# Kernel optimization log

Measured on AMD Instinct MI355X. Metric: run time of the kernel, lower is better.

The kernel has to match this reference:

```python
import jax, jax.numpy as jnp
import numpy as np

B, T, D, H = 4, 2048, 1024, 16
HD = D // H  # head_dim = 64


def setup_inputs() -> dict:
    key = jax.random.key(0)
    k1, k2, k3 = jax.random.split(key, 3)
    s = 0.02
    return {
        "x": jax.random.normal(k1, (B, T, D), dtype=jnp.float32),
        "qkv_w": jax.random.normal(k2, (D, 3 * D), dtype=jnp.float32) * s,
        "qkv_b": jnp.zeros((3 * D,), dtype=jnp.float32),
        "proj_w": jax.random.normal(k3, (D, D), dtype=jnp.float32) * s,
        "proj_b": jnp.zeros((D,), dtype=jnp.float32),
    }


def reference(x, qkv_w, qkv_b, proj_w, proj_b):
    b, t, d = x.shape
    qkv = x @ qkv_w + qkv_b                       # [B,T,3D]
    q, k, v = jnp.split(qkv, 3, axis=-1)
    # [B,T,D] -> [B,H,T,hd]
    q = q.reshape(b, t, H, HD).transpose(0, 2, 1, 3)
    k = k.reshape(b, t, H, HD).transpose(0, 2, 1, 3)
    v = v.reshape(b, t, H, HD).transpose(0, 2, 1, 3)
    att = jnp.einsum("bhqd,bhkd->bhqk", q, k) / np.sqrt(HD).astype(np.float32)
    causal = jnp.tril(jnp.ones((t, t), dtype=bool))
    att = jnp.where(causal[None, None], att, jnp.finfo(att.dtype).min)
    att = jax.nn.softmax(att, axis=-1)
    out = jnp.einsum("bhqk,bhkd->bhqd", att, v)   # [B,H,T,hd]
    out = out.transpose(0, 2, 1, 3).reshape(b, t, H * HD)
    out = out @ proj_w + proj_b                   # dropout p=0.0 -> identity
    return out
```

## Files before the change

kernel.cpp:

```cpp
#include <hip/hip_runtime.h>
#include <hip/hip_bf16.h>

#define Bsz 4
#define Tsz 2048
#define Dsz 1024
#define Hsz 16
#define HDsz 64

typedef __attribute__((ext_vector_type(8))) __bf16 bf16x8;
typedef __attribute__((ext_vector_type(4))) __bf16 bf16x4;
typedef __attribute__((ext_vector_type(4))) float f32x4;
typedef __attribute__((ext_vector_type(2))) float f32x2;
typedef unsigned short u16;
typedef unsigned int u32;

#define DEVI static __device__ __forceinline__

DEVI u16 f2bf(float f) {
    __bf16 h = (__bf16)f;
    union { __bf16 h; u16 u; } c; c.h = h; return c.u;
}
DEVI bf16x8 ld_bf8(const u16* p) { return *reinterpret_cast<const bf16x8*>(p); }

DEVI void gll16(const u16* g, u16* lds) {
    __builtin_amdgcn_global_load_lds(
        (const __attribute__((address_space(1))) u32*)g,
        (__attribute__((address_space(3))) u32*)lds, 16, 0, 0);
}

DEVI void mfma16(f32x4& c, f32x2 a, f32x2 b) {
    asm("v_mfma_f32_16x16x16_bf16 %0, %1, %2, %0" : "+v"(c) : "v"(a), "v"(b));
}

__global__ __launch_bounds__(256)
void conv_bf16(const float* __restrict__ X, u16* __restrict__ Xb)
{
    const size_t i = ((size_t)blockIdx.x * 256 + threadIdx.x) * 8;
    const float4 a = *(const float4*)(X + i);
    const float4 b = *(const float4*)(X + i + 4);
    u16 h[8] = { f2bf(a.x), f2bf(a.y), f2bf(a.z), f2bf(a.w),
                 f2bf(b.x), f2bf(b.y), f2bf(b.z), f2bf(b.w) };
    *(uint4*)(Xb + i) = *(uint4*)h;
}

__global__ __launch_bounds__(256)
void transpose_w(const float* __restrict__ W, u16* __restrict__ WT, int K, int N)
{
    __shared__ float tile[64][65];
    const int n0 = blockIdx.x * 64, k0 = blockIdx.y * 64;
    const int t = threadIdx.x;
    #pragma unroll
    for (int i = 0; i < 4; ++i) {
        const int idx = i*256 + t;
        const int row = idx >> 4, c4 = (idx & 15) * 4;
        const float4 v = *(const float4*)(W + (size_t)(k0 + row)*N + n0 + c4);
        tile[row][c4+0] = v.x; tile[row][c4+1] = v.y;
        tile[row][c4+2] = v.z; tile[row][c4+3] = v.w;
    }
    __syncthreads();
    #pragma unroll
    for (int j = 0; j < 2; ++j) {
        const int idx = j*256 + t;
        const int nr = idx >> 3, kc = (idx & 7) * 8;
        u16 h[8];
        #pragma unroll
        for (int e = 0; e < 8; ++e) h[e] = f2bf(tile[kc + e][nr]);
        *(uint4*)(WT + (size_t)(n0 + nr)*K + k0 + kc) = *(uint4*)h;
    }
}

template<int EPI>
__global__ __launch_bounds__(256, 3)
void gemm128(const u16* __restrict__ A, const u16* __restrict__ Bt,
             const float* __restrict__ bias, float* __restrict__ Cf,
             u16* __restrict__ Qo, u16* __restrict__ Ko, u16* __restrict__ Vo,
             int M, int N, int K)
{
    __shared__ u16 As[3][128][32];
    __shared__ u16 Bs[3][128][32];

    const int nx  = N >> 7;
    const int nwg = (int)gridDim.x;
    const int cpx = nwg >> 3;
    const int orig = blockIdx.x;
    const int bid  = (orig & 7) * cpx + (orig >> 3);
    const int tN = bid % nx, tM = bid / nx;

    const int t = threadIdx.x, l = t & 63, w = t >> 6;
    const int wm = w >> 1, wn = w & 1;
    const int lrow = l & 15, lk = l >> 4;

    f32x4 acc[4][4] = {};

    const u16* Ag = A  + (size_t)tM * 128 * K;
    const u16* Bg = Bt + (size_t)tN * 128 * K;

    int srow[2], sch[2];
    #pragma unroll
    for (int r = 0; r < 2; ++r) {
        const int c = r*256 + t;
        srow[r] = c >> 2;
        sch[r]  = (c & 3) ^ ((srow[r] >> 1) & 3);
    }
    const size_t ldso = (size_t)(t & 192) * 8;

    #define STAGE(buf, ks)                                                      \
        {                                                                       \
            _Pragma("unroll")                                                   \
            for (int r = 0; r < 2; ++r) {                                       \
                gll16(Ag + (size_t)srow[r]*K + (ks) + sch[r]*8,                 \
                      &As[buf][0][0] + (size_t)r*2048 + ldso);                  \
                gll16(Bg + (size_t)srow[r]*K + (ks) + sch[r]*8,                 \
                      &Bs[buf][0][0] + (size_t)r*2048 + ldso);                  \
            }                                                                   \
        }

    STAGE(0, 0);
    STAGE(1, 32);

    const int nk = K >> 5;
    int cur = 0;
    for (int i = 0; i < nk; ++i) {
        asm volatile("s_waitcnt vmcnt(4)" ::: "memory");
        __builtin_amdgcn_sched_barrier(0);
        __builtin_amdgcn_s_barrier();

        bf16x8 a[4], bb[4];
        #pragma unroll
        for (int ii = 0; ii < 4; ++ii) {
            const int ar = wm*64 + ii*16 + lrow;
            a[ii] = ld_bf8(&As[cur][ar][(lk ^ ((ar >> 1) & 3)) * 8]);
        }
        #pragma unroll
        for (int j = 0; j < 4; ++j) {
            const int br = wn*64 + j*16 + lrow;
            bb[j] = ld_bf8(&Bs[cur][br][(lk ^ ((br >> 1) & 3)) * 8]);
        }

        if (i + 2 < nk) {
            const int nb = (cur + 2) - ((cur + 2) >= 3 ? 3 : 0);
            STAGE(nb, (i + 2) * 32);
        }

        __builtin_amdgcn_s_setprio(1);
        #pragma unroll
        for (int ii = 0; ii < 4; ++ii)
        #pragma unroll
        for (int j = 0; j < 4; ++j)
            acc[ii][j] = __builtin_amdgcn_mfma_f32_16x16x32_bf16(a[ii], bb[j], acc[ii][j], 0, 0, 0);
        __builtin_amdgcn_s_setprio(0);

        cur = (cur + 1) - ((cur + 1) >= 3 ? 3 : 0);
    }
    #undef STAGE

    #pragma unroll
    for (int i = 0; i < 4; ++i)
    #pragma unroll
    for (int j = 0; j < 4; ++j)
    #pragma unroll
    for (int r = 0; r < 4; ++r) {
        const int row = tM*128 + wm*64 + i*16 + lk*4 + r;
        const int col = tN*128 + wn*64 + j*16 + lrow;
        const float v = acc[i][j][r] + bias[col];
        if (EPI == 0) {
            Cf[(size_t)row * N + col] = v;
        } else {
            const int which = col >> 10;
            const int h  = (col & 1023) >> 6;
            const int hd = col & 63;
            const int b  = row >> 11;
            const int tt = row & 2047;
            const int bh = b * Hsz + h;
            const u16 bv = f2bf(v);
            if (which == 0)      Qo[((size_t)bh * Tsz + tt) * HDsz + hd] = bv;
            else if (which == 1) Ko[((size_t)bh * Tsz + tt) * HDsz + hd] = bv;
            else                 Vo[((size_t)bh * HDsz + hd) * Tsz + tt] = bv;
        }
    }
}

__global__ __launch_bounds__(256, 4)
void attn3(const u16* __restrict__ Q, const u16* __restrict__ K,
           const u16* __restrict__ Vt, u16* __restrict__ AO)
{
    __shared__ u16 KV[2][2][64][64];

    const int y = blockIdx.y;
    const int x = blockIdx.x;
    const int idx = (x + (y >> 4)) & 15;
    const int qt = (idx & 1) ? (idx >> 1) : (15 - (idx >> 1));
    const int bh = y;
    const int t = threadIdx.x, w = t >> 6, l = t & 63;
    const int lrow = l & 15, lk = l >> 4;
    const int qw = qt*128 + w*32;
    const int qwmax = qw + 31;
    const int swz = lrow & 7;

    const u16* Qh = Q  + (size_t)bh * Tsz * HDsz;
    const u16* Kh = K  + (size_t)bh * Tsz * HDsz;
    const u16* Vh = Vt + (size_t)bh * HDsz * Tsz;

    bf16x8 qf[2][2];
    #pragma unroll
    for (int f = 0; f < 2; ++f)
    #pragma unroll
    for (int kh = 0; kh < 2; ++kh)
        qf[f][kh] = ld_bf8(&Qh[(size_t)(qw + f*16 + lrow)*HDsz + kh*32 + lk*8]);

    f32x4 o[2][4] = {};
    float m[2] = {-3e38f, -3e38f}, lsum[2] = {0.f, 0.f};

    const int ntile = 2*qt + 2;
    int cur = 0;

    #pragma unroll
    for (int rr = 0; rr < 2; ++rr) {
        const int c = rr*256 + t;
        const int row = c >> 3, gc = (c & 7) ^ (row & 7);
        gll16(Kh + (size_t)row*HDsz + gc*8,
              &KV[0][0][0][0] + (size_t)(rr*256 + (t & 192))*8);
        gll16(Vh + (size_t)row*Tsz + gc*8,
              &KV[0][1][0][0] + (size_t)(rr*256 + (t & 192))*8);
    }
    __syncthreads();

    for (int tk = 0; tk < ntile; ++tk) {
        if (tk + 1 < ntile) {
            const int nkv = (tk + 1) * 64;
            #pragma unroll
            for (int rr = 0; rr < 2; ++rr) {
                const int c = rr*256 + t;
                const int row = c >> 3, gc = (c & 7) ^ (row & 7);
                gll16(Kh + (size_t)(nkv + row)*HDsz + gc*8,
                      &KV[cur^1][0][0][0] + (size_t)(rr*256 + (t & 192))*8);
                gll16(Vh + (size_t)row*Tsz + nkv + gc*8,
                      &KV[cur^1][1][0][0] + (size_t)(rr*256 + (t & 192))*8);
            }
        }
        const int kv0 = tk * 64;
        if (kv0 <= qwmax) {
            const u16 (*Ks)[64] = KV[cur][0];
            const u16 (*Vs)[64] = KV[cur][1];
            const bool fullc    = (kv0 + 63 <= qwmax);
            const bool needmask = (kv0 + 63 > qw);

            f32x4 s[2][4];
            __builtin_amdgcn_s_setprio(1);
            #pragma unroll
            for (int c = 0; c < 4; ++c) {
                if (c >= 2 && !fullc) continue;
                const bf16x8 k0 = ld_bf8(&Ks[c*16 + lrow][((0 + lk) ^ swz) * 8]);
                const bf16x8 k1 = ld_bf8(&Ks[c*16 + lrow][((4 + lk) ^ swz) * 8]);
                #pragma unroll
                for (int f = 0; f < 2; ++f) {
                    f32x4 z = {};
                    z = __builtin_amdgcn_mfma_f32_16x16x32_bf16(k0, qf[f][0], z, 0, 0, 0);
                    z = __builtin_amdgcn_mfma_f32_16x16x32_bf16(k1, qf[f][1], z, 0, 0, 0);
                    s[f][c] = z;
                }
            }
            __builtin_amdgcn_s_setprio(0);

            #pragma unroll
            for (int f = 0; f < 2; ++f) {
                const int q = qw + f*16 + lrow;
                if (needmask) {
                    #pragma unroll
                    for (int c = 0; c < 4; ++c) {
                        if (c >= 2 && !fullc) continue;
                        const int base = kv0 + c*16 + lk*4;
                        #pragma unroll
                        for (int r = 0; r < 4; ++r)
                            if (base + r > q) s[f][c][r] = -1e30f;
                    }
                }
                f32x4 t01;
                #pragma unroll
                for (int r = 0; r < 4; ++r) {
                    t01[r] = fmaxf(s[f][0][r], s[f][1][r]);
                    if (fullc) t01[r] = fmaxf(t01[r], fmaxf(s[f][2][r], s[f][3][r]));
                }
                float mx = fmaxf(fmaxf(t01[0], t01[1]), fmaxf(t01[2], t01[3]));
                mx = fmaxf(mx, __shfl_xor(mx, 16));
                mx = fmaxf(mx, __shfl_xor(mx, 32));
                if (__any(mx > m[f] + 64.f)) {
                    const float mn = fmaxf(m[f], mx);
                    const float al = __expf((m[f] - mn) * 0.125f);
                    lsum[f] *= al;
                    m[f] = mn;
                    #pragma unroll
                    for (int c = 0; c < 4; ++c)
                    #pragma unroll
                    for (int r = 0; r < 4; ++r) o[f][c][r] *= al;
                }
                const float nm8 = -m[f] * 0.125f;
                f32x4 ps4 = {};
                #pragma unroll
                for (int c = 0; c < 4; ++c) {
                    if (c >= 2 && !fullc) continue;
                    #pragma unroll
                    for (int r = 0; r < 4; ++r) {
                        const float p = __expf(fmaf(s[f][c][r], 0.125f, nm8));
                        s[f][c][r] = p;
                        ps4[r] += p;
                    }
                }
                float ps = (ps4[0] + ps4[1]) + (ps4[2] + ps4[3]);
                ps += __shfl_xor(ps, 16);
                ps += __shfl_xor(ps, 32);
                lsum[f] += ps;
            }

            __builtin_amdgcn_s_setprio(1);
            #pragma unroll
            for (int c = 0; c < 4; ++c) {
                if (c >= 2 && !fullc) continue;
                union { bf16x4 v; f32x2 f; } p0, p1;
                #pragma unroll
                for (int r = 0; r < 4; ++r) {
                    p0.v[r] = (__bf16)s[0][c][r];
                    p1.v[r] = (__bf16)s[1][c][r];
                }
                #pragma unroll
                for (int chd = 0; chd < 4; ++chd) {
                    const f32x2 va = *reinterpret_cast<const f32x2*>(
                        &Vs[chd*16 + lrow][(((c*2 + (lk >> 1)) ^ swz) << 3) + ((lk & 1) << 2)]);
                    mfma16(o[0][chd], va, p0.f);
                    mfma16(o[1][chd], va, p1.f);
                }
            }
            __builtin_amdgcn_s_setprio(0);
        }
        __syncthreads();
        cur ^= 1;
    }

    const int b = bh >> 4, h = bh & 15;
    #pragma unroll
    for (int f = 0; f < 2; ++f) {
        const float rl = 1.0f / lsum[f];
        #pragma unroll
        for (int chd = 0; chd < 4; ++chd) {
            u16 ov[4] = { f2bf(o[f][chd][0]*rl), f2bf(o[f][chd][1]*rl),
                          f2bf(o[f][chd][2]*rl), f2bf(o[f][chd][3]*rl) };
            *(ushort4*)(AO + ((size_t)(b*Tsz + qw + f*16 + lrow))*Dsz
                           + h*HDsz + chd*16 + lk*4) = *(ushort4*)ov;
        }
    }
}

extern "C" void kernel_launch(void* const* d_in, const int* in_sizes, int n_in,
                              void* d_out, int out_size, void* d_ws, size_t ws_size,
                              hipStream_t stream)
{
    (void)in_sizes; (void)n_in; (void)out_size; (void)ws_size;

    const float* x      = (const float*)d_in[0];
    const float* qkv_w  = (const float*)d_in[1];
    const float* qkv_b  = (const float*)d_in[2];
    const float* proj_w = (const float*)d_in[3];
    const float* proj_b = (const float*)d_in[4];
    float* out = (float*)d_out;

    char* ws = (char*)d_ws;
    const size_t SZ = (size_t)Bsz * Hsz * Tsz * HDsz * sizeof(u16);
    u16* R0 = (u16*)(ws);
    u16* Qb = (u16*)(ws + SZ);
    u16* Kb = (u16*)(ws + 2*SZ);
    u16* Vt = (u16*)(ws + 3*SZ);
    u16* WQKVT = R0;
    u16* AO    = R0;
    u16* WPT   = Qb;

    u16* Xb = (u16*)d_out;

    const int M = Bsz * Tsz;

    conv_bf16<<<(M*Dsz)/(256*8), 256, 0, stream>>>(x, Xb);
    transpose_w<<<dim3(3*Dsz/64, Dsz/64), 256, 0, stream>>>(qkv_w, WQKVT, Dsz, 3*Dsz);
    gemm128<1><<<dim3((3*Dsz/128) * (M/128)), 256, 0, stream>>>(
        Xb, WQKVT, qkv_b, nullptr, Qb, Kb, Vt, M, 3*Dsz, Dsz);
    attn3<<<dim3(Tsz/128, Bsz*Hsz), 256, 0, stream>>>(Qb, Kb, Vt, AO);
    transpose_w<<<dim3(Dsz/64, Dsz/64), 256, 0, stream>>>(proj_w, WPT, Dsz, Dsz);
    gemm128<0><<<dim3((Dsz/128) * (M/128)), 256, 0, stream>>>(
        AO, WPT, proj_b, out, nullptr, nullptr, nullptr, M, Dsz, Dsz);
}
```

Baseline: 201.6 us.

## Replace 128x128 GEMM with 256x256 tiled 8-wave GEMM using ping-pong quadrant schedule

Both projection GEMMs now use 256x256 output tiles with 512 threads (8 waves, 2x4 layout), a K-step of 64, and double-buffered LDS split into row halves. The main loop is split into four quadrant phases, with barriers between them and global-to-LDS prefetches spread across the phases, so loads overlap MFMA work. The aim is to raise arithmetic intensity and cut global and LDS traffic per FLOP. In exchange, the grid shrinks (only 128 blocks for the output projection, fewer than the CU count), register pressure rises, and there are more barriers per iteration.

```diff
diff --git a/kernel.cpp b/kernel.cpp
--- a/kernel.cpp
+++ b/kernel.cpp
@@ -70,98 +70,177 @@
 }
 
 template<int EPI>
-__global__ __launch_bounds__(256, 3)
-void gemm128(const u16* __restrict__ A, const u16* __restrict__ Bt,
+__global__ __launch_bounds__(512, 2)
+void gemm256(const u16* __restrict__ A, const u16* __restrict__ Bt,
              const float* __restrict__ bias, float* __restrict__ Cf,
              u16* __restrict__ Qo, u16* __restrict__ Ko, u16* __restrict__ Vo,
              int M, int N, int K)
 {
-    __shared__ u16 As[3][128][32];
-    __shared__ u16 Bs[3][128][32];
-
-    const int nx  = N >> 7;
+    __shared__ u16 Ash[2][2][128*64];
+    __shared__ u16 Bsh[2][2][128*64];
+
+    const int nx  = N >> 8;
     const int nwg = (int)gridDim.x;
     const int cpx = nwg >> 3;
-    const int orig = blockIdx.x;
+    const int orig = (int)blockIdx.x;
     const int bid  = (orig & 7) * cpx + (orig >> 3);
     const int tN = bid % nx, tM = bid / nx;
 
-    const int t = threadIdx.x, l = t & 63, w = t >> 6;
-    const int wm = w >> 1, wn = w & 1;
+    const int t = (int)threadIdx.x, l = t & 63, w = t >> 6;
+    const int wm = w >> 2, wn = w & 3;
     const int lrow = l & 15, lk = l >> 4;
 
-    f32x4 acc[4][4] = {};
-
-    const u16* Ag = A  + (size_t)tM * 128 * K;
-    const u16* Bg = Bt + (size_t)tN * 128 * K;
-
-    int srow[2], sch[2];
+    f32x4 acc[8][4] = {};
+
+    const u16* Ag = A  + (size_t)tM * 256 * K;
+    const u16* Bg = Bt + (size_t)tN * 256 * K;
+
+    int strow[2], scol[2];
     #pragma unroll
     for (int r = 0; r < 2; ++r) {
-        const int c = r*256 + t;
-        srow[r] = c >> 2;
-        sch[r]  = (c & 3) ^ ((srow[r] >> 1) & 3);
-    }
-    const size_t ldso = (size_t)(t & 192) * 8;
-
-    #define STAGE(buf, ks)                                                      \
-        {                                                                       \
-            _Pragma("unroll")                                                   \
-            for (int r = 0; r < 2; ++r) {                                       \
-                gll16(Ag + (size_t)srow[r]*K + (ks) + sch[r]*8,                 \
-                      &As[buf][0][0] + (size_t)r*2048 + ldso);                  \
-                gll16(Bg + (size_t)srow[r]*K + (ks) + sch[r]*8,                 \
-                      &Bs[buf][0][0] + (size_t)r*2048 + ldso);                  \
-            }                                                                   \
-        }
-
-    STAGE(0, 0);
-    STAGE(1, 32);
-
-    const int nk = K >> 5;
-    int cur = 0;
-    for (int i = 0; i < nk; ++i) {
-        asm volatile("s_waitcnt vmcnt(4)" ::: "memory");
-        __builtin_amdgcn_sched_barrier(0);
-        __builtin_amdgcn_s_barrier();
-
-        bf16x8 a[4], bb[4];
-        #pragma unroll
-        for (int ii = 0; ii < 4; ++ii) {
-            const int ar = wm*64 + ii*16 + lrow;
-            a[ii] = ld_bf8(&As[cur][ar][(lk ^ ((ar >> 1) & 3)) * 8]);
-        }
-        #pragma unroll
-        for (int j = 0; j < 4; ++j) {
-            const int br = wn*64 + j*16 + lrow;
-            bb[j] = ld_bf8(&Bs[cur][br][(lk ^ ((br >> 1) & 3)) * 8]);
-        }
-
-        if (i + 2 < nk) {
-            const int nb = (cur + 2) - ((cur + 2) >= 3 ? 3 : 0);
-            STAGE(nb, (i + 2) * 32);
-        }
-
+        const int c = r*512 + t;
+        strow[r] = c >> 3;
+        scol[r]  = (((c & 7) ^ ((strow[r] >> 1) & 7)) << 3);
+    }
+    const size_t ldso = (size_t)(t & 448) * 8;
+
+#define STG(buf, isB, half, kt) {                                              \
+    const u16* g0_ = (isB ? Bg : Ag) + ((size_t)(half)*128 + strow[0])*K + (kt) + scol[0]; \
+    const u16* g1_ = (isB ? Bg : Ag) + ((size_t)(half)*128 + strow[1])*K + (kt) + scol[1]; \
+    u16* lp_ = (isB ? Bsh[buf][half] : Ash[buf][half]);                        \
+    gll16(g0_, lp_ + ldso);                                                    \
+    gll16(g1_, lp_ + 4096 + ldso); }
+
+#define SWZ(r_, ch_) ((r_)*64 + ((((ch_) ^ (((r_) >> 1) & 7))) << 3))
+
+    const int nt = K >> 6;
+
+    STG(0,0,0,0) STG(0,0,1,0) STG(0,1,0,0) STG(0,1,1,0)
+    STG(1,1,0,64) STG(1,1,1,64)
+    asm volatile("s_waitcnt vmcnt(4)" ::: "memory");
+    __builtin_amdgcn_sched_barrier(0);
+    __builtin_amdgcn_s_barrier();
+    __builtin_amdgcn_sched_barrier(0);
+
+    for (int tt = 0; tt < nt; ++tt) {
+        const int buf = tt & 1;
+        const int kt = tt << 6;
+        const u16* Ahalf = Ash[buf][wm];
+        const u16* Bhalf = Bsh[buf][wn >> 1];
+        const int brow = (wn & 1) * 64;
+
+        bf16x8 Alo[4][2], Ahi[4][2], Blo[2][2], Bhi[2][2];
+
+        #pragma unroll
+        for (int ii = 0; ii < 4; ++ii)
+        #pragma unroll
+        for (int kk = 0; kk < 2; ++kk) {
+            const int r_ = ii*16 + lrow;
+            Alo[ii][kk] = ld_bf8(&Ahalf[SWZ(r_, kk*4 + lk)]);
+        }
+        #pragma unroll
+        for (int jj = 0; jj < 2; ++jj)
+        #pragma unroll
+        for (int kk = 0; kk < 2; ++kk) {
+            const int r_ = brow + jj*16 + lrow;
+            Blo[jj][kk] = ld_bf8(&Bhalf[SWZ(r_, kk*4 + lk)]);
+        }
+        if (tt + 1 < nt) STG(buf^1, 0, 0, kt+64)
+        __builtin_amdgcn_sched_barrier(0);
+        __builtin_amdgcn_s_barrier();
+        __builtin_amdgcn_sched_barrier(0);
         __builtin_amdgcn_s_setprio(1);
         #pragma unroll
         for (int ii = 0; ii < 4; ++ii)
         #pragma unroll
-        for (int j = 0; j < 4; ++j)
-            acc[ii][j] = __builtin_amdgcn_mfma_f32_16x16x32_bf16(a[ii], bb[j], acc[ii][j], 0, 0, 0);
+        for (int jj = 0; jj < 2; ++jj)
+        #pragma unroll
+        for (int kk = 0; kk < 2; ++kk)
+            acc[ii][jj] = __builtin_amdgcn_mfma_f32_16x16x32_bf16(
+                Alo[ii][kk], Blo[jj][kk], acc[ii][jj], 0, 0, 0);
         __builtin_amdgcn_s_setprio(0);
-
-        cur = (cur + 1) - ((cur + 1) >= 3 ? 3 : 0);
-    }
-    #undef STAGE
-
-    #pragma unroll
-    for (int i = 0; i < 4; ++i)
+        __builtin_amdgcn_sched_barrier(0);
+        __builtin_amdgcn_s_barrier();
+        __builtin_amdgcn_sched_barrier(0);
+
+        #pragma unroll
+        for (int jj = 0; jj < 2; ++jj)
+        #pragma unroll
+        for (int kk = 0; kk < 2; ++kk) {
+            const int r_ = brow + 32 + jj*16 + lrow;
+            Bhi[jj][kk] = ld_bf8(&Bhalf[SWZ(r_, kk*4 + lk)]);
+        }
+        if (tt + 1 < nt) STG(buf^1, 0, 1, kt+64)
+        __builtin_amdgcn_sched_barrier(0);
+        __builtin_amdgcn_s_barrier();
+        __builtin_amdgcn_sched_barrier(0);
+        __builtin_amdgcn_s_setprio(1);
+        #pragma unroll
+        for (int ii = 0; ii < 4; ++ii)
+        #pragma unroll
+        for (int jj = 0; jj < 2; ++jj)
+        #pragma unroll
+        for (int kk = 0; kk < 2; ++kk)
+            acc[ii][2+jj] = __builtin_amdgcn_mfma_f32_16x16x32_bf16(
+                Alo[ii][kk], Bhi[jj][kk], acc[ii][2+jj], 0, 0, 0);
+        __builtin_amdgcn_s_setprio(0);
+        __builtin_amdgcn_sched_barrier(0);
+        __builtin_amdgcn_s_barrier();
+        __builtin_amdgcn_sched_barrier(0);
+
+        #pragma unroll
+        for (int ii = 0; ii < 4; ++ii)
+        #pragma unroll
+        for (int kk = 0; kk < 2; ++kk) {
+            const int r_ = 64 + ii*16 + lrow;
+            Ahi[ii][kk] = ld_bf8(&Ahalf[SWZ(r_, kk*4 + lk)]);
+        }
+        if (tt + 2 < nt) STG(buf, 1, 0, kt+128)
+        __builtin_amdgcn_sched_barrier(0);
+        __builtin_amdgcn_s_barrier();
+        __builtin_amdgcn_sched_barrier(0);
+        __builtin_amdgcn_s_setprio(1);
+        #pragma unroll
+        for (int ii = 0; ii < 4; ++ii)
+        #pragma unroll
+        for (int jj = 0; jj < 2; ++jj)
+        #pragma unroll
+        for (int kk = 0; kk < 2; ++kk)
+            acc[4+ii][jj] = __builtin_amdgcn_mfma_f32_16x16x32_bf16(
+                Ahi[ii][kk], Blo[jj][kk], acc[4+ii][jj], 0, 0, 0);
+        __builtin_amdgcn_s_setprio(0);
+        __builtin_amdgcn_sched_barrier(0);
+        __builtin_amdgcn_s_barrier();
+        __builtin_amdgcn_sched_barrier(0);
+
+        if (tt + 2 < nt) STG(buf, 1, 1, kt+128)
+        __builtin_amdgcn_s_setprio(1);
+        #pragma unroll
+        for (int ii = 0; ii < 4; ++ii)
+        #pragma unroll
+        for (int jj = 0; jj < 2; ++jj)
+        #pragma unroll
+        for (int kk = 0; kk < 2; ++kk)
+            acc[4+ii][2+jj] = __builtin_amdgcn_mfma_f32_16x16x32_bf16(
+                Ahi[ii][kk], Bhi[jj][kk], acc[4+ii][2+jj], 0, 0, 0);
+        __builtin_amdgcn_s_setprio(0);
+        if (tt + 2 < nt) { asm volatile("s_waitcnt vmcnt(4)" ::: "memory"); }
+        else             { asm volatile("s_waitcnt vmcnt(0)" ::: "memory"); }
+        __builtin_amdgcn_sched_barrier(0);
+        __builtin_amdgcn_s_barrier();
+        __builtin_amdgcn_sched_barrier(0);
+    }
+#undef STG
+#undef SWZ
+
+    #pragma unroll
+    for (int i = 0; i < 8; ++i)
     #pragma unroll
     for (int j = 0; j < 4; ++j)
     #pragma unroll
     for (int r = 0; r < 4; ++r) {
-        const int row = tM*128 + wm*64 + i*16 + lk*4 + r;
-        const int col = tN*128 + wn*64 + j*16 + lrow;
+        const int row = tM*256 + wm*128 + i*16 + lk*4 + r;
+        const int col = tN*256 + wn*64 + j*16 + lrow;
         const float v = acc[i][j][r] + bias[col];
         if (EPI == 0) {
             Cf[(size_t)row * N + col] = v;
@@ -379,10 +458,10 @@
 
     conv_bf16<<<(M*Dsz)/(256*8), 256, 0, stream>>>(x, Xb);
     transpose_w<<<dim3(3*Dsz/64, Dsz/64), 256, 0, stream>>>(qkv_w, WQKVT, Dsz, 3*Dsz);
-    gemm128<1><<<dim3((3*Dsz/128) * (M/128)), 256, 0, stream>>>(
+    gemm256<1><<<dim3((M/256) * (3*Dsz/256)), 512, 0, stream>>>(
         Xb, WQKVT, qkv_b, nullptr, Qb, Kb, Vt, M, 3*Dsz, Dsz);
     attn3<<<dim3(Tsz/128, Bsz*Hsz), 256, 0, stream>>>(Qb, Kb, Vt, AO);
     transpose_w<<<dim3(Dsz/64, Dsz/64), 256, 0, stream>>>(proj_w, WPT, Dsz, Dsz);
-    gemm128<0><<<dim3((Dsz/128) * (M/128)), 256, 0, stream>>>(
+    gemm256<0><<<dim3((M/256) * (Dsz/256)), 512, 0, stream>>>(
         AO, WPT, proj_b, out, nullptr, nullptr, nullptr, M, Dsz, Dsz);
 }
```

New measurement: 224.7 us. 11.5% more time.

## Remap GEMM tiles per XCD by column and vectorize transposed V epilogue stores

Applied to the files above, without the earlier changes.

Changes the workgroup-to-tile mapping so each XCD owns a contiguous band of N tiles, which keeps the weight (B) tiles resident in that XCD's L2 instead of spreading M rows. The last k-iteration now waits with vmcnt(0) so the final stage is fully loaded. The epilogue hoists the bias load and writes the transposed V output as packed 4-element ushort4 stores instead of scattered 2-byte stores. The new mapping relies on nx being divisible by 8, and it changes how A tiles are reused across XCDs.

```diff
diff --git a/kernel.cpp b/kernel.cpp
--- a/kernel.cpp
+++ b/kernel.cpp
@@ -80,11 +80,11 @@
     __shared__ u16 Bs[3][128][32];
 
     const int nx  = N >> 7;
-    const int nwg = (int)gridDim.x;
-    const int cpx = nwg >> 3;
-    const int orig = blockIdx.x;
-    const int bid  = (orig & 7) * cpx + (orig >> 3);
-    const int tN = bid % nx, tM = bid / nx;
+    const int q   = nx >> 3;
+    const int xcd = blockIdx.x & 7;
+    const int c   = blockIdx.x >> 3;
+    const int tN  = xcd * q + (q > 1 ? (c % q) : 0);
+    const int tM  = (q > 1 ? (c / q) : c);
 
     const int t = threadIdx.x, l = t & 63, w = t >> 6;
     const int wm = w >> 1, wn = w & 1;
@@ -98,9 +98,9 @@
     int srow[2], sch[2];
     #pragma unroll
     for (int r = 0; r < 2; ++r) {
-        const int c = r*256 + t;
-        srow[r] = c >> 2;
-        sch[r]  = (c & 3) ^ ((srow[r] >> 1) & 3);
+        const int cc = r*256 + t;
+        srow[r] = cc >> 2;
+        sch[r]  = (cc & 3) ^ ((srow[r] >> 1) & 3);
     }
     const size_t ldso = (size_t)(t & 192) * 8;
 
@@ -121,7 +121,8 @@
     const int nk = K >> 5;
     int cur = 0;
     for (int i = 0; i < nk; ++i) {
-        asm volatile("s_waitcnt vmcnt(4)" ::: "memory");
+        if (i + 1 < nk) { asm volatile("s_waitcnt vmcnt(4)" ::: "memory"); }
+        else            { asm volatile("s_waitcnt vmcnt(0)" ::: "memory"); }
         __builtin_amdgcn_sched_barrier(0);
         __builtin_amdgcn_s_barrier();
 
@@ -157,25 +158,35 @@
     #pragma unroll
     for (int i = 0; i < 4; ++i)
     #pragma unroll
-    for (int j = 0; j < 4; ++j)
-    #pragma unroll
-    for (int r = 0; r < 4; ++r) {
-        const int row = tM*128 + wm*64 + i*16 + lk*4 + r;
-        const int col = tN*128 + wn*64 + j*16 + lrow;
-        const float v = acc[i][j][r] + bias[col];
+    for (int j = 0; j < 4; ++j) {
+        const int row0 = tM*128 + wm*64 + i*16 + lk*4;
+        const int col  = tN*128 + wn*64 + j*16 + lrow;
+        const float bv = bias[col];
         if (EPI == 0) {
-            Cf[(size_t)row * N + col] = v;
+            #pragma unroll
+            for (int r = 0; r < 4; ++r)
+                Cf[(size_t)(row0 + r) * N + col] = acc[i][j][r] + bv;
         } else {
             const int which = col >> 10;
             const int h  = (col & 1023) >> 6;
             const int hd = col & 63;
-            const int b  = row >> 11;
-            const int tt = row & 2047;
-            const int bh = b * Hsz + h;
-            const u16 bv = f2bf(v);
-            if (which == 0)      Qo[((size_t)bh * Tsz + tt) * HDsz + hd] = bv;
-            else if (which == 1) Ko[((size_t)bh * Tsz + tt) * HDsz + hd] = bv;
-            else                 Vo[((size_t)bh * HDsz + hd) * Tsz + tt] = bv;
+            if (which == 2) {
+                const int b  = row0 >> 11;
+                const int tt = row0 & 2047;
+                const int bh = b * Hsz + h;
+                u16 pk[4] = { f2bf(acc[i][j][0] + bv), f2bf(acc[i][j][1] + bv),
+                              f2bf(acc[i][j][2] + bv), f2bf(acc[i][j][3] + bv) };
+                *(ushort4*)(Vo + ((size_t)bh * HDsz + hd) * Tsz + tt) = *(ushort4*)pk;
+            } else {
+                u16* P = (which == 0) ? Qo : Ko;
+                #pragma unroll
+                for (int r = 0; r < 4; ++r) {
+                    const int row = row0 + r;
+                    const int bh  = (row >> 11) * Hsz + h;
+                    P[((size_t)bh * Tsz + (row & 2047)) * HDsz + hd] =
+                        f2bf(acc[i][j][r] + bv);
+                }
+            }
         }
     }
 }
```

Measured after the change: 194.4 us, median of 4. -3.5%, faster.
